# Kernel optimization log

Hardware: AMD Instinct MI355X
Metric: run time of the kernel (lower is better)

The kernel has to match this reference:

```python
import jax, jax.numpy as jnp
import numpy as np

N, F, H, C, E, K = 50000, 512, 512, 256, 800000, 1024


def _linear_params(key, fan_in, fan_out):
    kw, kb = jax.random.split(key)
    s = 1.0 / np.sqrt(fan_in)
    W = jax.random.uniform(kw, (fan_out, fan_in), jnp.float32, -s, s)
    b = jax.random.uniform(kb, (fan_out,), jnp.float32, -s, s)
    return W, b


def setup_inputs() -> dict:
    key = jax.random.key(0)
    ks = jax.random.split(key, 8)
    W1, b1 = _linear_params(ks[0], F, H)
    W2, b2 = _linear_params(ks[1], H, H)
    W3, b3 = _linear_params(ks[2], H, C)
    Wfc, bfc = _linear_params(ks[3], C, F)
    x = jax.random.normal(ks[4], (N, F), jnp.float32)
    edge_index = jax.random.randint(ks[5], (2, E), 0, N, jnp.int32)
    central_idx = jnp.sort(jax.random.randint(ks[6], (K,), 0, N, jnp.int32))
    zero = jnp.zeros((), jnp.float32)  # train_eps=True initialises eps=0
    return {
        "x": x, "edge_index": edge_index, "central_idx": central_idx,
        "W1": W1, "b1": b1, "eps1": zero,
        "W2": W2, "b2": b2, "eps2": zero,
        "W3": W3, "b3": b3, "eps3": zero,
        "Wfc": Wfc, "bfc": bfc,
    }


def _leaky_relu(v):
    return jnp.where(v >= 0, v, 0.2 * v)


def _gin_layer(h, edge_index, W, b, eps):
    # sum over neighbors (src -> dst); explicit self-loops add one extra h_i,
    # so total center coefficient is (1 + eps) + 1 = (2 + eps)
    n = h.shape[0]
    agg = jax.ops.segment_sum(h[edge_index[0]], edge_index[1], num_segments=n)
    return (agg + (2.0 + eps) * h) @ W.T + b


def reference(x, edge_index, central_idx, W1, b1, eps1, W2, b2, eps2,
              W3, b3, eps3, Wfc, bfc):
    h = _leaky_relu(_gin_layer(x, edge_index, W1, b1, eps1))
    h = _leaky_relu(_gin_layer(h, edge_index, W2, b2, eps2))
    x3 = _leaky_relu(_gin_layer(h, edge_index, W3, b3, eps3))
    # fc(x)[central_node_mask] == fc(x[central_idx]) for a mask with ones at central_idx
    out = x3[central_idx] @ Wfc.T + bfc
    return (x3, out)
```

## Files before the change

kernel.cpp:

```cpp
#include <hip/hip_runtime.h>
#include <stdint.h>

typedef unsigned short u16;
typedef __attribute__((ext_vector_type(4))) unsigned short u16x4;
typedef __attribute__((ext_vector_type(8))) unsigned short u16x8;
typedef __attribute__((ext_vector_type(8))) short bf16x8;
typedef __attribute__((ext_vector_type(4))) float f32x4;
typedef __attribute__((ext_vector_type(4))) float f4v;
typedef __attribute__((ext_vector_type(4))) int i32x4;

__device__ __forceinline__ float b2f(u16 u) {
    union { unsigned u; float f; } c; c.u = ((unsigned)u) << 16; return c.f;
}
__device__ __forceinline__ u16 f2b(float f) {
    union { float f; unsigned u; } c; c.f = f;
    unsigned r = c.u + 0x7fffu + ((c.u >> 16) & 1u);
    return (u16)(r >> 16);
}

__device__ __forceinline__ void gload16(const void* g, void* l) {
    __builtin_amdgcn_global_load_lds(
        (const __attribute__((address_space(1))) unsigned int*)g,
        (__attribute__((address_space(3))) unsigned int*)l, 16, 0, 0);
}

__device__ __forceinline__ void cvt4(const float* in, u16* out, int idx) {
    f4v v = ((const f4v*)in)[idx];
    u16x4 o;
    o[0] = f2b(v[0]); o[1] = f2b(v[1]); o[2] = f2b(v[2]); o[3] = f2b(v[3]);
    ((u16x4*)out)[idx] = o;
}

__device__ __forceinline__ float cvt_ub0(unsigned v) { float f; asm("v_cvt_f32_ubyte0 %0, %1" : "=v"(f) : "v"(v)); return f; }
__device__ __forceinline__ float cvt_ub1(unsigned v) { float f; asm("v_cvt_f32_ubyte1 %0, %1" : "=v"(f) : "v"(v)); return f; }
__device__ __forceinline__ float cvt_ub2(unsigned v) { float f; asm("v_cvt_f32_ubyte2 %0, %1" : "=v"(f) : "v"(v)); return f; }
__device__ __forceinline__ float cvt_ub3(unsigned v) { float f; asm("v_cvt_f32_ubyte3 %0, %1" : "=v"(f) : "v"(v)); return f; }

__device__ __forceinline__ void dq_accu(int2 d, float s, float* acc) {
    unsigned ux = (unsigned)d.x ^ 0x80808080u;
    unsigned uy = (unsigned)d.y ^ 0x80808080u;
    acc[0] = fmaf(s, cvt_ub0(ux), acc[0]);
    acc[1] = fmaf(s, cvt_ub1(ux), acc[1]);
    acc[2] = fmaf(s, cvt_ub2(ux), acc[2]);
    acc[3] = fmaf(s, cvt_ub3(ux), acc[3]);
    acc[4] = fmaf(s, cvt_ub0(uy), acc[4]);
    acc[5] = fmaf(s, cvt_ub1(uy), acc[5]);
    acc[6] = fmaf(s, cvt_ub2(uy), acc[6]);
    acc[7] = fmaf(s, cvt_ub3(uy), acc[7]);
}
__device__ __forceinline__ void dq_accu4(int d, float s, float* acc) {
    unsigned ux = (unsigned)d ^ 0x80808080u;
    acc[0] = fmaf(s, cvt_ub0(ux), acc[0]);
    acc[1] = fmaf(s, cvt_ub1(ux), acc[1]);
    acc[2] = fmaf(s, cvt_ub2(ux), acc[2]);
    acc[3] = fmaf(s, cvt_ub3(ux), acc[3]);
}

__device__ __forceinline__ void qrow512(const float* __restrict__ src, char* __restrict__ dst,
                                        float* __restrict__ srow, int r, int lane) {
    const f4v* p = (const f4v*)(src + (size_t)r * 512) + lane * 2;
    f4v v0 = p[0], v1 = p[1];
    float m = 0.f;
#pragma unroll
    for (int j = 0; j < 4; j++) { m = fmaxf(m, fabsf(v0[j])); m = fmaxf(m, fabsf(v1[j])); }
#pragma unroll
    for (int d = 1; d < 64; d <<= 1) m = fmaxf(m, __shfl_xor(m, d));
    float qs = (m > 0.f) ? 127.f / m : 0.f;
    int lo = 0, hi = 0;
#pragma unroll
    for (int j = 0; j < 4; j++) { int q = (int)rintf(v0[j] * qs); lo |= (q & 0xFF) << (8 * j); }
#pragma unroll
    for (int j = 0; j < 4; j++) { int q = (int)rintf(v1[j] * qs); hi |= (q & 0xFF) << (8 * j); }
    ((int2*)(dst + (size_t)r * 512))[lane] = make_int2(lo, hi);
    if (lane == 0) srow[r] = (m > 0.f) ? m / 127.f : 0.f;
}

__global__ void prep_kernel(const float* __restrict__ x, char* __restrict__ qx,
                            float* __restrict__ xs,
                            const float* __restrict__ W1, char* __restrict__ W1q, float* __restrict__ ws1,
                            const float* __restrict__ W2, char* __restrict__ W2q, float* __restrict__ ws2,
                            const float* __restrict__ W3, u16* __restrict__ W3b,
                            const int* __restrict__ ei, int* __restrict__ deg, int E) {
    int b = blockIdx.x;
    int tid = threadIdx.x;
    if (b < 12500) {
        int w = b * 4 + (tid >> 6);
        int lane = tid & 63;
        const f4v* xr = (const f4v*)(x + (size_t)w * 512) + lane * 2;
        f4v v0 = xr[0], v1 = xr[1];
        float m = 0.f;
#pragma unroll
        for (int j = 0; j < 4; j++) { m = fmaxf(m, fabsf(v0[j])); m = fmaxf(m, fabsf(v1[j])); }
#pragma unroll
        for (int d = 1; d < 8; d <<= 1) m = fmaxf(m, __shfl_xor(m, d));
        float scale = (m > 0.f) ? 127.f / m : 0.f;
        int lo = 0, hi = 0;
#pragma unroll
        for (int j = 0; j < 4; j++) { int q = (int)rintf(v0[j] * scale); lo |= (q & 0xFF) << (8 * j); }
#pragma unroll
        for (int j = 0; j < 4; j++) { int q = (int)rintf(v1[j] * scale); hi |= (q & 0xFF) << (8 * j); }
        ((int2*)(qx + (size_t)w * 512))[lane] = make_int2(lo, hi);
        if ((lane & 7) == 0) xs[w * 8 + (lane >> 3)] = (m > 0.f) ? m / 127.f : 0.f;
    } else if (b < 12628) {
        qrow512(W1, W1q, ws1, (b - 12500) * 4 + (tid >> 6), tid & 63);
    } else if (b < 12756) {
        qrow512(W2, W2q, ws2, (b - 12628) * 4 + (tid >> 6), tid & 63);
    } else if (b < 12884) {
        cvt4(W3, W3b, (b - 12756) * 256 + tid);
    } else {
        int e = (b - 12884) * 256 + tid;
        if (e < E) atomicAdd(&deg[ei[E + e]], 1);
    }
}

__global__ void scanA_kernel(const int* __restrict__ deg, int* __restrict__ bsum, int n) {
    __shared__ int sm[256];
    int tid = threadIdx.x;
    int i = blockIdx.x * 256 + tid;
    sm[tid] = (i < n) ? deg[i] : 0;
    __syncthreads();
#pragma unroll
    for (int off = 128; off > 0; off >>= 1) {
        if (tid < off) sm[tid] += sm[tid + off];
        __syncthreads();
    }
    if (tid == 0) bsum[blockIdx.x] = sm[0];
}

__global__ void scanB_kernel(int* __restrict__ bsum, int nb) {
    __shared__ int sm[256];
    int tid = threadIdx.x;
    int v = (tid < nb) ? bsum[tid] : 0;
    sm[tid] = v;
    __syncthreads();
#pragma unroll
    for (int off = 1; off < 256; off <<= 1) {
        int t = (tid >= off) ? sm[tid - off] : 0;
        __syncthreads();
        sm[tid] += t;
        __syncthreads();
    }
    if (tid < nb) bsum[tid] = sm[tid] - v;
}

__global__ void scanC_kernel(const int* __restrict__ deg, const int* __restrict__ bsum,
                             int* __restrict__ rowp, int n) {
    __shared__ int sm[256];
    int tid = threadIdx.x;
    int b = blockIdx.x;
    int i = b * 256 + tid;
    int v = (i < n) ? deg[i] : 0;
    sm[tid] = v;
    __syncthreads();
#pragma unroll
    for (int off = 1; off < 256; off <<= 1) {
        int t = (tid >= off) ? sm[tid - off] : 0;
        __syncthreads();
        sm[tid] += t;
        __syncthreads();
    }
    if (i < n) rowp[i] = bsum[b] + sm[tid] - v;
    if (i == n - 1) rowp[n] = bsum[b] + sm[tid];
}

__global__ void fill_kernel(const int* __restrict__ ei, const int* __restrict__ rowp,
                            int* __restrict__ cnt, int* __restrict__ col, int E) {
    int e = blockIdx.x * blockDim.x + threadIdx.x;
    if (e < E) {
        int dst = ei[E + e];
        int pos = atomicAdd(&cnt[dst], 1);
        col[rowp[dst] + pos] = ei[e];
    }
}

__global__ void agg_q512(const char* __restrict__ q, const float* __restrict__ sc,
                         char* __restrict__ tq, float* __restrict__ tsc,
                         const int* __restrict__ rowp, const int* __restrict__ col,
                         const float* __restrict__ epsp, int N) {
    int w = (blockIdx.x * blockDim.x + threadIdx.x) >> 6;
    if (w >= N) return;
    int lane = threadIdx.x & 63;
    float coef = 2.0f + epsp[0];
    const int2* base = (const int2*)q;
    int ch = lane >> 3;
    float acc[8];
#pragma unroll
    for (int j = 0; j < 8; j++) acc[j] = 0.f;
    float csum = 0.f;
    {
        float s = coef * sc[w * 8 + ch];
        csum += s;
        dq_accu(base[(size_t)w * 64 + lane], s, acc);
    }
    int p = rowp[w], e = rowp[w + 1];
    for (; p + 2 <= e; p += 2) {
        int s0 = __builtin_amdgcn_readfirstlane(col[p]);
        int s1 = __builtin_amdgcn_readfirstlane(col[p + 1]);
        int2 v0 = base[(size_t)s0 * 64 + lane];
        int2 v1 = base[(size_t)s1 * 64 + lane];
        float f0 = sc[s0 * 8 + ch];
        float f1 = sc[s1 * 8 + ch];
        csum += f0 + f1;
        dq_accu(v0, f0, acc);
        dq_accu(v1, f1, acc);
    }
    if (p < e) {
        int s0 = __builtin_amdgcn_readfirstlane(col[p]);
        float f0 = sc[s0 * 8 + ch];
        csum += f0;
        dq_accu(base[(size_t)s0 * 64 + lane], f0, acc);
    }
    float corr = 128.f * csum;
#pragma unroll
    for (int j = 0; j < 8; j++) acc[j] -= corr;
    float m = 0.f;
#pragma unroll
    for (int j = 0; j < 8; j++) m = fmaxf(m, fabsf(acc[j]));
#pragma unroll
    for (int d = 1; d < 64; d <<= 1) m = fmaxf(m, __shfl_xor(m, d));
    float qs = (m > 0.f) ? 127.f / m : 0.f;
    int lo = 0, hi = 0;
#pragma unroll
    for (int j = 0; j < 4; j++) { int qv = (int)rintf(acc[j] * qs); lo |= (qv & 0xFF) << (8 * j); }
#pragma unroll
    for (int j = 0; j < 4; j++) { int qv = (int)rintf(acc[j + 4] * qs); hi |= (qv & 0xFF) << (8 * j); }
    ((int2*)(tq + (size_t)w * 512))[lane] = make_int2(lo, hi);
    if (lane == 0) tsc[w] = (m > 0.f) ? m / 127.f : 0.f;
}

__global__ void agg3_q(const char* __restrict__ q, const float* __restrict__ sc,
                       float* __restrict__ out, const int* __restrict__ rowp,
                       const int* __restrict__ col, const float* __restrict__ epsp,
                       const float* __restrict__ bias, int N) {
    int w = (blockIdx.x * blockDim.x + threadIdx.x) >> 6;
    if (w >= N) return;
    int lane = threadIdx.x & 63;
    float coef = 2.0f + epsp[0];
    const int* base = (const int*)q;
    int ch = lane >> 4;
    f4v bv = *(const f4v*)(bias + lane * 4);
    float acc[4];
#pragma unroll
    for (int j = 0; j < 4; j++) acc[j] = 0.f;
    float csum = 0.f;
    {
        float s = coef * sc[w * 4 + ch];
        csum += s;
        dq_accu4(base[(size_t)w * 64 + lane], s, acc);
    }
    int p = rowp[w], e = rowp[w + 1];
    for (; p + 2 <= e; p += 2) {
        int s0 = __builtin_amdgcn_readfirstlane(col[p]);
        int s1 = __builtin_amdgcn_readfirstlane(col[p + 1]);
        int v0 = base[(size_t)s0 * 64 + lane];
        int v1 = base[(size_t)s1 * 64 + lane];
        float f0 = sc[s0 * 4 + ch];
        float f1 = sc[s1 * 4 + ch];
        csum += f0 + f1;
        dq_accu4(v0, f0, acc);
        dq_accu4(v1, f1, acc);
    }
    if (p < e) {
        int s0 = __builtin_amdgcn_readfirstlane(col[p]);
        float f0 = sc[s0 * 4 + ch];
        csum += f0;
        dq_accu4(base[(size_t)s0 * 64 + lane], f0, acc);
    }
    float corr = 128.f * csum;
    f4v o;
#pragma unroll
    for (int j = 0; j < 4; j++) {
        float v = acc[j] - corr + bv[j];
        o[j] = (v >= 0.f) ? v : 0.2f * v;
    }
    *(f4v*)(out + (size_t)w * 256 + lane * 4) = o;
}

template <int MODE>
__launch_bounds__(256)
__global__ void gemm_i8_kernel(const char* __restrict__ A, const float* __restrict__ sA,
                               const char* __restrict__ Wq, const float* __restrict__ sW,
                               const float* __restrict__ bias, u16* __restrict__ C,
                               char* __restrict__ qc, float* __restrict__ scw,
                               int M, int Nout, int K, int nby) {
    int nwg = gridDim.x;
    int orig = blockIdx.x;
    int q8 = nwg >> 3, r8 = nwg & 7;
    int xcd = orig & 7, idx = orig >> 3;
    int wgid = (xcd < r8 ? xcd * (q8 + 1) : r8 * (q8 + 1) + (xcd - r8) * q8) + idx;
    int by = wgid % nby;
    int bx = wgid / nby;

    __shared__ alignas(16) char lA[2][128 * 64];
    __shared__ alignas(16) char lB[2][128 * 64];
    int tid = threadIdx.x;
    int lane = tid & 63;
    int wv = tid >> 6;
    int m0 = bx * 128;
    int n0 = by * 128;
    int wrow = (wv >> 1) * 64;
    int wcol = (wv & 1) * 64;

    i32x4 acc[4][4];
#pragma unroll
    for (int i = 0; i < 4; i++)
#pragma unroll
        for (int j = 0; j < 4; j++) acc[i][j] = (i32x4){0, 0, 0, 0};

    int srow = lane >> 2;
    int scol = (lane & 3) * 16;
    int arow0 = m0 + wv * 16 + srow;        if (arow0 >= M) arow0 = M - 1;
    int arow1 = m0 + 64 + wv * 16 + srow;   if (arow1 >= M) arow1 = M - 1;
    const char* gA0 = A + (size_t)arow0 * K + scol;
    const char* gA1 = A + (size_t)arow1 * K + scol;
    const char* gB0 = Wq + (size_t)(n0 + wv * 16 + srow) * K + scol;
    const char* gB1 = Wq + (size_t)(n0 + 64 + wv * 16 + srow) * K + scol;
    int la0 = (wv * 16) * 64;
    int la1 = (64 + wv * 16) * 64;

    int fr = lane & 15;
    int kq = (lane >> 4) * 16;
    int nt = K / 64;

    gload16(gA0, lA[0] + la0);
    gload16(gA1, lA[0] + la1);
    gload16(gB0, lB[0] + la0);
    gload16(gB1, lB[0] + la1);
    __syncthreads();

    for (int t = 0; t < nt; t++) {
        int cur = t & 1;
        if (t + 1 < nt) {
            int kt = (t + 1) * 64;
            gload16(gA0 + kt, lA[cur ^ 1] + la0);
            gload16(gA1 + kt, lA[cur ^ 1] + la1);
            gload16(gB0 + kt, lB[cur ^ 1] + la0);
            gload16(gB1 + kt, lB[cur ^ 1] + la1);
        }
        i32x4 af[4], bf[4];
#pragma unroll
        for (int m = 0; m < 4; m++)
            af[m] = *(const i32x4*)(lA[cur] + (wrow + m * 16 + fr) * 64 + kq);
#pragma unroll
        for (int nf = 0; nf < 4; nf++)
            bf[nf] = *(const i32x4*)(lB[cur] + (wcol + nf * 16 + fr) * 64 + kq);
#pragma unroll
        for (int m = 0; m < 4; m++)
#pragma unroll
            for (int nf = 0; nf < 4; nf++)
                acc[m][nf] = __builtin_amdgcn_mfma_i32_16x16x64_i8(af[m], bf[nf], acc[m][nf], 0, 0, 0);
        __syncthreads();
    }

    int r0 = (lane >> 4) * 4;
#pragma unroll
    for (int m = 0; m < 4; m++) {
        float sa[4];
#pragma unroll
        for (int r = 0; r < 4; r++) {
            int gr = m0 + wrow + m * 16 + r0 + r;
            sa[r] = sA[gr < M ? gr : M - 1];
        }
        float v[4][4];
#pragma unroll
        for (int nf = 0; nf < 4; nf++) {
            int gc = n0 + wcol + nf * 16 + fr;
            float swv = sW[gc];
            float bv = bias[gc];
#pragma unroll
            for (int r = 0; r < 4; r++) {
                float tv = (float)acc[m][nf][r] * sa[r] * swv + bv;
                v[nf][r] = (tv >= 0.f) ? tv : 0.2f * tv;
            }
        }
        if constexpr (MODE == 1) {
#pragma unroll
            for (int nf = 0; nf < 4; nf++) {
                int gc = n0 + wcol + nf * 16 + fr;
#pragma unroll
                for (int r = 0; r < 4; r++) {
                    int gr = m0 + wrow + m * 16 + r0 + r;
                    if (gr < M) C[(size_t)gr * Nout + gc] = f2b(v[nf][r]);
                }
            }
        } else {
            int nch = Nout >> 6;
            int chunk = (n0 + wcol) >> 6;
#pragma unroll
            for (int r = 0; r < 4; r++) {
                float amax = fmaxf(fmaxf(fabsf(v[0][r]), fabsf(v[1][r])),
                                   fmaxf(fabsf(v[2][r]), fabsf(v[3][r])));
#pragma unroll
                for (int d = 1; d < 16; d <<= 1) amax = fmaxf(amax, __shfl_xor(amax, d));
                int gr = m0 + wrow + m * 16 + r0 + r;
                float scale = (amax > 0.f) ? 127.f / amax : 0.f;
                if (gr < M) {
#pragma unroll
                    for (int nf = 0; nf < 4; nf++) {
                        int qv = (int)rintf(v[nf][r] * scale);
                        qc[(size_t)gr * Nout + n0 + wcol + nf * 16 + fr] = (signed char)qv;
                    }
                    if (fr == 0)
                        scw[(size_t)gr * nch + chunk] = (amax > 0.f) ? amax / 127.f : 0.f;
                }
            }
        }
    }
}

#define BM 128
#define BN 128
#define BK 32

__launch_bounds__(256)
__global__ void gemm_bt_kernel(const u16* __restrict__ A, const u16* __restrict__ W,
                               char* __restrict__ qc, float* __restrict__ scw,
                               int M, int Nout, int K, int nby) {
    int nwg = gridDim.x;
    int orig = blockIdx.x;
    int q8 = nwg >> 3, r8 = nwg & 7;
    int xcd = orig & 7, idx = orig >> 3;
    int wgid = (xcd < r8 ? xcd * (q8 + 1) : r8 * (q8 + 1) + (xcd - r8) * q8) + idx;
    int by = wgid % nby;
    int bx = wgid / nby;

    __shared__ alignas(16) u16 lA[2][BM * BK];
    __shared__ alignas(16) u16 lB[2][BN * BK];
    int tid = threadIdx.x;
    int lane = tid & 63;
    int wv = tid >> 6;
    int m0 = bx * BM;
    int n0 = by * BN;
    int wrow = (wv >> 1) * 64;
    int wcol = (wv & 1) * 64;

    f32x4 acc[4][4];
#pragma unroll
    for (int i = 0; i < 4; i++)
#pragma unroll
        for (int j = 0; j < 4; j++) acc[i][j] = (f32x4){0.f, 0.f, 0.f, 0.f};

    int srow = lane >> 2;
    int scol = (lane & 3) * 8;
    int arow0 = m0 + wv * 16 + srow;        if (arow0 >= M) arow0 = M - 1;
    int arow1 = m0 + 64 + wv * 16 + srow;   if (arow1 >= M) arow1 = M - 1;
    const u16* gA0 = A + (size_t)arow0 * K + scol;
    const u16* gA1 = A + (size_t)arow1 * K + scol;
    const u16* gB0 = W + (size_t)(n0 + wv * 16 + srow) * K + scol;
    const u16* gB1 = W + (size_t)(n0 + 64 + wv * 16 + srow) * K + scol;
    int la0 = (wv * 16) * BK;
    int la1 = (64 + wv * 16) * BK;

    int fr = lane & 15;
    int kq = (lane >> 4) * 8;
    int nt = K / BK;

    gload16(gA0, lA[0] + la0);
    gload16(gA1, lA[0] + la1);
    gload16(gB0, lB[0] + la0);
    gload16(gB1, lB[0] + la1);
    __syncthreads();

    for (int t = 0; t < nt; t++) {
        int cur = t & 1;
        if (t + 1 < nt) {
            int kt = (t + 1) * BK;
            gload16(gA0 + kt, lA[cur ^ 1] + la0);
            gload16(gA1 + kt, lA[cur ^ 1] + la1);
            gload16(gB0 + kt, lB[cur ^ 1] + la0);
            gload16(gB1 + kt, lB[cur ^ 1] + la1);
        }
        bf16x8 af[4], bfr[4];
#pragma unroll
        for (int m = 0; m < 4; m++)
            af[m] = *(const bf16x8*)(lA[cur] + (wrow + m * 16 + fr) * BK + kq);
#pragma unroll
        for (int nf = 0; nf < 4; nf++)
            bfr[nf] = *(const bf16x8*)(lB[cur] + (wcol + nf * 16 + fr) * BK + kq);
#pragma unroll
        for (int m = 0; m < 4; m++)
#pragma unroll
            for (int nf = 0; nf < 4; nf++)
                acc[m][nf] = __builtin_amdgcn_mfma_f32_16x16x32_bf16(af[m], bfr[nf], acc[m][nf], 0, 0, 0);
        __syncthreads();
    }

    int r0 = (lane >> 4) * 4;
    int nch = Nout >> 6;
    int chunk = (n0 + wcol) >> 6;
#pragma unroll
    for (int m = 0; m < 4; m++) {
        float v[4][4];
#pragma unroll
        for (int nf = 0; nf < 4; nf++)
#pragma unroll
            for (int r = 0; r < 4; r++) v[nf][r] = acc[m][nf][r];
#pragma unroll
        for (int r = 0; r < 4; r++) {
            float amax = fmaxf(fmaxf(fabsf(v[0][r]), fabsf(v[1][r])),
                               fmaxf(fabsf(v[2][r]), fabsf(v[3][r])));
#pragma unroll
            for (int d = 1; d < 16; d <<= 1) amax = fmaxf(amax, __shfl_xor(amax, d));
            int gr = m0 + wrow + m * 16 + r0 + r;
            float scale = (amax > 0.f) ? 127.f / amax : 0.f;
            if (gr < M) {
#pragma unroll
                for (int nf = 0; nf < 4; nf++) {
                    int qv = (int)rintf(v[nf][r] * scale);
                    qc[(size_t)gr * Nout + n0 + wcol + nf * 16 + fr] = (signed char)qv;
                }
                if (fr == 0)
                    scw[(size_t)gr * nch + chunk] = (amax > 0.f) ? amax / 127.f : 0.f;
            }
        }
    }
}

__global__ void fc_kernel(const float* __restrict__ x3, const int* __restrict__ cidx,
                          const float* __restrict__ W, const float* __restrict__ b,
                          float* __restrict__ out, int C, int F, int Kc) {
    __shared__ float xr[8][256];
    int base = blockIdx.x * 8;
    int tid = threadIdx.x;
#pragma unroll
    for (int j = 0; j < 8; j++) {
        int k = base + j;
        if (k < Kc) xr[j][tid] = x3[(size_t)cidx[k] * C + tid];
    }
    __syncthreads();
    for (int f = tid; f < F; f += 256) {
        const float4* wr = (const float4*)(W + (size_t)f * C);
        float acc[8];
#pragma unroll
        for (int j = 0; j < 8; j++) acc[j] = 0.f;
        for (int c4 = 0; c4 < C / 4; ++c4) {
            float4 wv = wr[c4];
#pragma unroll
            for (int j = 0; j < 8; j++) {
                acc[j] += xr[j][c4 * 4 + 0] * wv.x + xr[j][c4 * 4 + 1] * wv.y +
                          xr[j][c4 * 4 + 2] * wv.z + xr[j][c4 * 4 + 3] * wv.w;
            }
        }
        float bf = b[f];
#pragma unroll
        for (int j = 0; j < 8; j++) {
            int k = base + j;
            if (k < Kc) out[(size_t)k * F + f] = acc[j] + bf;
        }
    }
}

extern "C" void kernel_launch(void* const* d_in, const int* in_sizes, int n_in,
                              void* d_out, int out_size, void* d_ws, size_t ws_size,
                              hipStream_t stream) {
    const float* x    = (const float*)d_in[0];
    const int*   ei   = (const int*)d_in[1];
    const int*   cidx = (const int*)d_in[2];
    const float* W1   = (const float*)d_in[3];
    const float* b1   = (const float*)d_in[4];
    const float* eps1 = (const float*)d_in[5];
    const float* W2   = (const float*)d_in[6];
    const float* b2   = (const float*)d_in[7];
    const float* eps2 = (const float*)d_in[8];
    const float* W3   = (const float*)d_in[9];
    const float* b3   = (const float*)d_in[10];
    const float* eps3 = (const float*)d_in[11];
    const float* Wfc  = (const float*)d_in[12];
    const float* bfc  = (const float*)d_in[13];

    const int F = 512, H = 512, Cc = 256;
    const int Nn = in_sizes[0] / F;
    const int E  = in_sizes[1] / 2;
    const int Kc = in_sizes[2];

    const size_t SZ_Q = (size_t)Nn * 512;
    char* ws = (char*)d_ws;
    char*  tq   = ws;
    char*  qbuf = ws + SZ_Q;
    float* tsc  = (float*)(ws + 2 * SZ_Q);
    float* sc   = tsc + Nn;
    char*  W1q  = (char*)(sc + (size_t)Nn * 8);
    float* ws1  = (float*)(W1q + 262144);
    char*  W2q  = (char*)(ws1 + 512);
    float* ws2  = (float*)(W2q + 262144);
    u16*   W3b  = (u16*)(ws2 + 512);
    int*   deg  = (int*)((char*)W3b + 262144);
    int*   cnt  = deg + Nn;
    int*   rowp = cnt + Nn;
    int*   colx = rowp + Nn + 1;
    int*   bsum = colx + E;

    u16* hbuf = (u16*)d_out;

    int nbScan = (Nn + 255) / 256;

    hipMemsetAsync(deg, 0, 2 * (size_t)Nn * sizeof(int), stream);
    int prepBlocks = 12884 + (E + 255) / 256;
    prep_kernel<<<prepBlocks, 256, 0, stream>>>(x, qbuf, sc, W1, W1q, ws1, W2, W2q, ws2,
                                                W3, W3b, ei, deg, E);
    scanA_kernel<<<nbScan, 256, 0, stream>>>(deg, bsum, Nn);
    scanB_kernel<<<1, 256, 0, stream>>>(bsum, nbScan);
    scanC_kernel<<<nbScan, 256, 0, stream>>>(deg, bsum, rowp, Nn);
    fill_kernel<<<(E + 255) / 256, 256, 0, stream>>>(ei, rowp, cnt, colx, E);

    int aggBlocks = (Nn * 64 + 255) / 256;
    int nbx = (Nn + 127) / 128;

    agg_q512<<<aggBlocks, 256, 0, stream>>>(qbuf, sc, tq, tsc, rowp, colx, eps1, Nn);
    gemm_i8_kernel<2><<<nbx * 4, 256, 0, stream>>>(tq, tsc, W1q, ws1, b1, nullptr,
                                                   qbuf, sc, Nn, H, F, 4);
    agg_q512<<<aggBlocks, 256, 0, stream>>>(qbuf, sc, tq, tsc, rowp, colx, eps2, Nn);
    gemm_i8_kernel<1><<<nbx * 4, 256, 0, stream>>>(tq, tsc, W2q, ws2, b2, hbuf,
                                                   nullptr, nullptr, Nn, H, H, 4);
    gemm_bt_kernel<<<nbx * 2, 256, 0, stream>>>(hbuf, W3b, qbuf, sc, Nn, Cc, H, 2);
    float* x3 = (float*)d_out;
    agg3_q<<<aggBlocks, 256, 0, stream>>>(qbuf, sc, x3, rowp, colx, eps3, b3, Nn);

    float* outp = x3 + (size_t)Nn * Cc;
    fc_kernel<<<(Kc + 7) / 8, 256, 0, stream>>>(x3, cidx, Wfc, bfc, outp, Cc, F, Kc);
}
```

Baseline: 451.5 us.

## Store quantized features in 64-column chunk planes and split aggregation per chunk

The int8 feature buffers move to a chunk-major layout: one plane of 64 columns per chunk, each row 64 bytes. Aggregation kernels launch one block slice per chunk, which shrinks the gather footprint per pass so it can stay cache-resident. Each wavefront also processes eight edges in parallel and reduces them with shuffles, instead of walking edges serially. The 512-wide aggregation now writes bf16 and needs a separate requantization kernel, which adds a pass and extra memory traffic. Edge-parallel lanes also waste work on padded slots when degree is low.

```diff
diff --git a/kernel.cpp b/kernel.cpp
--- a/kernel.cpp
+++ b/kernel.cpp
@@ -48,13 +48,6 @@
     acc[6] = fmaf(s, cvt_ub2(uy), acc[6]);
     acc[7] = fmaf(s, cvt_ub3(uy), acc[7]);
 }
-__device__ __forceinline__ void dq_accu4(int d, float s, float* acc) {
-    unsigned ux = (unsigned)d ^ 0x80808080u;
-    acc[0] = fmaf(s, cvt_ub0(ux), acc[0]);
-    acc[1] = fmaf(s, cvt_ub1(ux), acc[1]);
-    acc[2] = fmaf(s, cvt_ub2(ux), acc[2]);
-    acc[3] = fmaf(s, cvt_ub3(ux), acc[3]);
-}
 
 __device__ __forceinline__ void qrow512(const float* __restrict__ src, char* __restrict__ dst,
                                         float* __restrict__ srow, int r, int lane) {
@@ -75,12 +68,12 @@
     if (lane == 0) srow[r] = (m > 0.f) ? m / 127.f : 0.f;
 }
 
-__global__ void prep_kernel(const float* __restrict__ x, char* __restrict__ qx,
+__global__ void prep_kernel(const float* __restrict__ x, char* __restrict__ qxT,
                             float* __restrict__ xs,
                             const float* __restrict__ W1, char* __restrict__ W1q, float* __restrict__ ws1,
                             const float* __restrict__ W2, char* __restrict__ W2q, float* __restrict__ ws2,
                             const float* __restrict__ W3, u16* __restrict__ W3b,
-                            const int* __restrict__ ei, int* __restrict__ deg, int E) {
+                            const int* __restrict__ ei, int* __restrict__ deg, int E, int N) {
     int b = blockIdx.x;
     int tid = threadIdx.x;
     if (b < 12500) {
@@ -99,7 +92,7 @@
         for (int j = 0; j < 4; j++) { int q = (int)rintf(v0[j] * scale); lo |= (q & 0xFF) << (8 * j); }
 #pragma unroll
         for (int j = 0; j < 4; j++) { int q = (int)rintf(v1[j] * scale); hi |= (q & 0xFF) << (8 * j); }
-        ((int2*)(qx + (size_t)w * 512))[lane] = make_int2(lo, hi);
+        ((int2*)qxT)[((size_t)(lane >> 3) * N + w) * 8 + (lane & 7)] = make_int2(lo, hi);
         if ((lane & 7) == 0) xs[w * 8 + (lane >> 3)] = (m > 0.f) ? m / 127.f : 0.f;
     } else if (b < 12628) {
         qrow512(W1, W1q, ws1, (b - 12500) * 4 + (tid >> 6), tid & 63);
@@ -173,107 +166,126 @@
     }
 }
 
-__global__ void agg_q512(const char* __restrict__ q, const float* __restrict__ sc,
-                         char* __restrict__ tq, float* __restrict__ tsc,
-                         const int* __restrict__ rowp, const int* __restrict__ col,
-                         const float* __restrict__ epsp, int N) {
-    int w = (blockIdx.x * blockDim.x + threadIdx.x) >> 6;
+__global__ void agg_t512(const char* __restrict__ qT, const float* __restrict__ sc,
+                         u16* __restrict__ t, const int* __restrict__ rowp,
+                         const int* __restrict__ col, const float* __restrict__ epsp, int N) {
+    int tid = threadIdx.x;
+    int c = blockIdx.x & 7;
+    int w = (blockIdx.x >> 3) * 4 + (tid >> 6);
     if (w >= N) return;
-    int lane = threadIdx.x & 63;
+    int lane = tid & 63;
+    int slot = lane >> 3;
+    int fo = lane & 7;
+    const int2* plane = (const int2*)qT + (size_t)c * N * 8;
     float coef = 2.0f + epsp[0];
-    const int2* base = (const int2*)q;
-    int ch = lane >> 3;
     float acc[8];
 #pragma unroll
     for (int j = 0; j < 8; j++) acc[j] = 0.f;
     float csum = 0.f;
-    {
-        float s = coef * sc[w * 8 + ch];
+    if (slot == 0) {
+        float s = coef * sc[w * 8 + c];
         csum += s;
-        dq_accu(base[(size_t)w * 64 + lane], s, acc);
-    }
-    int p = rowp[w], e = rowp[w + 1];
-    for (; p + 2 <= e; p += 2) {
-        int s0 = __builtin_amdgcn_readfirstlane(col[p]);
-        int s1 = __builtin_amdgcn_readfirstlane(col[p + 1]);
-        int2 v0 = base[(size_t)s0 * 64 + lane];
-        int2 v1 = base[(size_t)s1 * 64 + lane];
-        float f0 = sc[s0 * 8 + ch];
-        float f1 = sc[s1 * 8 + ch];
-        csum += f0 + f1;
-        dq_accu(v0, f0, acc);
-        dq_accu(v1, f1, acc);
-    }
-    if (p < e) {
-        int s0 = __builtin_amdgcn_readfirstlane(col[p]);
-        float f0 = sc[s0 * 8 + ch];
-        csum += f0;
-        dq_accu(base[(size_t)s0 * 64 + lane], f0, acc);
-    }
-    float corr = 128.f * csum;
-#pragma unroll
-    for (int j = 0; j < 8; j++) acc[j] -= corr;
-    float m = 0.f;
-#pragma unroll
-    for (int j = 0; j < 8; j++) m = fmaxf(m, fabsf(acc[j]));
-#pragma unroll
-    for (int d = 1; d < 64; d <<= 1) m = fmaxf(m, __shfl_xor(m, d));
-    float qs = (m > 0.f) ? 127.f / m : 0.f;
-    int lo = 0, hi = 0;
-#pragma unroll
-    for (int j = 0; j < 4; j++) { int qv = (int)rintf(acc[j] * qs); lo |= (qv & 0xFF) << (8 * j); }
-#pragma unroll
-    for (int j = 0; j < 4; j++) { int qv = (int)rintf(acc[j + 4] * qs); hi |= (qv & 0xFF) << (8 * j); }
-    ((int2*)(tq + (size_t)w * 512))[lane] = make_int2(lo, hi);
-    if (lane == 0) tsc[w] = (m > 0.f) ? m / 127.f : 0.f;
-}
-
-__global__ void agg3_q(const char* __restrict__ q, const float* __restrict__ sc,
+        dq_accu(plane[(size_t)w * 8 + fo], s, acc);
+    }
+    int p0 = rowp[w], p1 = rowp[w + 1];
+    for (int p = p0; p < p1; p += 8) {
+        int e = p + slot;
+        int ec = (e < p1) ? e : p1 - 1;
+        int src = col[ec];
+        float s = (e < p1) ? sc[src * 8 + c] : 0.f;
+        csum += s;
+        dq_accu(plane[(size_t)src * 8 + fo], s, acc);
+    }
+#pragma unroll
+    for (int d = 8; d < 64; d <<= 1) {
+        csum += __shfl_xor(csum, d);
+#pragma unroll
+        for (int j = 0; j < 8; j++) acc[j] += __shfl_xor(acc[j], d);
+    }
+    if (slot == 0) {
+        float corr = 128.f * csum;
+        u16x8 o;
+#pragma unroll
+        for (int j = 0; j < 8; j++) o[j] = f2b(acc[j] - corr);
+        *(u16x8*)(t + (size_t)w * 512 + c * 64 + fo * 8) = o;
+    }
+}
+
+__global__ void agg3_t(const char* __restrict__ qT, const float* __restrict__ sc,
                        float* __restrict__ out, const int* __restrict__ rowp,
                        const int* __restrict__ col, const float* __restrict__ epsp,
                        const float* __restrict__ bias, int N) {
-    int w = (blockIdx.x * blockDim.x + threadIdx.x) >> 6;
+    int tid = threadIdx.x;
+    int x8 = blockIdx.x & 7;
+    int c = x8 >> 1;
+    int w = (blockIdx.x >> 3) * 8 + (x8 & 1) * 4 + (tid >> 6);
     if (w >= N) return;
+    int lane = tid & 63;
+    int slot = lane >> 3;
+    int fo = lane & 7;
+    const int2* plane = (const int2*)qT + (size_t)c * N * 8;
+    float coef = 2.0f + epsp[0];
+    float acc[8];
+#pragma unroll
+    for (int j = 0; j < 8; j++) acc[j] = 0.f;
+    float csum = 0.f;
+    if (slot == 0) {
+        float s = coef * sc[w * 4 + c];
+        csum += s;
+        dq_accu(plane[(size_t)w * 8 + fo], s, acc);
+    }
+    int p0 = rowp[w], p1 = rowp[w + 1];
+    for (int p = p0; p < p1; p += 8) {
+        int e = p + slot;
+        int ec = (e < p1) ? e : p1 - 1;
+        int src = col[ec];
+        float s = (e < p1) ? sc[src * 4 + c] : 0.f;
+        csum += s;
+        dq_accu(plane[(size_t)src * 8 + fo], s, acc);
+    }
+#pragma unroll
+    for (int d = 8; d < 64; d <<= 1) {
+        csum += __shfl_xor(csum, d);
+#pragma unroll
+        for (int j = 0; j < 8; j++) acc[j] += __shfl_xor(acc[j], d);
+    }
+    if (slot == 0) {
+        float corr = 128.f * csum;
+        int f0 = c * 64 + fo * 8;
+        f4v o0, o1;
+#pragma unroll
+        for (int j = 0; j < 4; j++) {
+            float v = acc[j] - corr + bias[f0 + j];
+            o0[j] = (v >= 0.f) ? v : 0.2f * v;
+        }
+#pragma unroll
+        for (int j = 0; j < 4; j++) {
+            float v = acc[j + 4] - corr + bias[f0 + 4 + j];
+            o1[j] = (v >= 0.f) ? v : 0.2f * v;
+        }
+        *(f4v*)(out + (size_t)w * 256 + f0) = o0;
+        *(f4v*)(out + (size_t)w * 256 + f0 + 4) = o1;
+    }
+}
+
+__global__ void requant512(const u16* __restrict__ h, char* __restrict__ qh,
+                           float* __restrict__ hs) {
+    int w = blockIdx.x * 4 + (threadIdx.x >> 6);
     int lane = threadIdx.x & 63;
-    float coef = 2.0f + epsp[0];
-    const int* base = (const int*)q;
-    int ch = lane >> 4;
-    f4v bv = *(const f4v*)(bias + lane * 4);
-    float acc[4];
-#pragma unroll
-    for (int j = 0; j < 4; j++) acc[j] = 0.f;
-    float csum = 0.f;
-    {
-        float s = coef * sc[w * 4 + ch];
-        csum += s;
-        dq_accu4(base[(size_t)w * 64 + lane], s, acc);
-    }
-    int p = rowp[w], e = rowp[w + 1];
-    for (; p + 2 <= e; p += 2) {
-        int s0 = __builtin_amdgcn_readfirstlane(col[p]);
-        int s1 = __builtin_amdgcn_readfirstlane(col[p + 1]);
-        int v0 = base[(size_t)s0 * 64 + lane];
-        int v1 = base[(size_t)s1 * 64 + lane];
-        float f0 = sc[s0 * 4 + ch];
-        float f1 = sc[s1 * 4 + ch];
-        csum += f0 + f1;
-        dq_accu4(v0, f0, acc);
-        dq_accu4(v1, f1, acc);
-    }
-    if (p < e) {
-        int s0 = __builtin_amdgcn_readfirstlane(col[p]);
-        float f0 = sc[s0 * 4 + ch];
-        csum += f0;
-        dq_accu4(base[(size_t)s0 * 64 + lane], f0, acc);
-    }
-    float corr = 128.f * csum;
-    f4v o;
-#pragma unroll
-    for (int j = 0; j < 4; j++) {
-        float v = acc[j] - corr + bv[j];
-        o[j] = (v >= 0.f) ? v : 0.2f * v;
-    }
-    *(f4v*)(out + (size_t)w * 256 + lane * 4) = o;
+    u16x8 v = ((const u16x8*)(h + (size_t)w * 512))[lane];
+    float f[8]; float m = 0.f;
+#pragma unroll
+    for (int j = 0; j < 8; j++) { f[j] = b2f(v[j]); m = fmaxf(m, fabsf(f[j])); }
+#pragma unroll
+    for (int d = 1; d < 64; d <<= 1) m = fmaxf(m, __shfl_xor(m, d));
+    float scale = (m > 0.f) ? 127.f / m : 0.f;
+    int lo = 0, hi = 0;
+#pragma unroll
+    for (int j = 0; j < 4; j++) { int q = (int)rintf(f[j] * scale); lo |= (q & 0xFF) << (8 * j); }
+#pragma unroll
+    for (int j = 0; j < 4; j++) { int q = (int)rintf(f[j + 4] * scale); hi |= (q & 0xFF) << (8 * j); }
+    ((int2*)(qh + (size_t)w * 512))[lane] = make_int2(lo, hi);
+    if (lane == 0) hs[w] = (m > 0.f) ? m / 127.f : 0.f;
 }
 
 template <int MODE>
@@ -398,7 +410,7 @@
 #pragma unroll
                     for (int nf = 0; nf < 4; nf++) {
                         int qv = (int)rintf(v[nf][r] * scale);
-                        qc[(size_t)gr * Nout + n0 + wcol + nf * 16 + fr] = (signed char)qv;
+                        qc[((size_t)chunk * M + gr) * 64 + (nf * 16 + fr)] = (signed char)qv;
                     }
                     if (fr == 0)
                         scw[(size_t)gr * nch + chunk] = (amax > 0.f) ? amax / 127.f : 0.f;
@@ -507,7 +519,7 @@
 #pragma unroll
                 for (int nf = 0; nf < 4; nf++) {
                     int qv = (int)rintf(v[nf][r] * scale);
-                    qc[(size_t)gr * Nout + n0 + wcol + nf * 16 + fr] = (signed char)qv;
+                    qc[((size_t)chunk * M + gr) * 64 + (nf * 16 + fr)] = (signed char)qv;
                 }
                 if (fr == 0)
                     scw[(size_t)gr * nch + chunk] = (amax > 0.f) ? amax / 127.f : 0.f;
@@ -575,9 +587,10 @@
 
     const size_t SZ_Q = (size_t)Nn * 512;
     char* ws = (char*)d_ws;
-    char*  tq   = ws;
-    char*  qbuf = ws + SZ_Q;
-    float* tsc  = (float*)(ws + 2 * SZ_Q);
+    u16*   bufT = (u16*)ws;
+    char*  tq   = ws + 2 * SZ_Q;
+    char*  qbuf = ws + 3 * SZ_Q;
+    float* tsc  = (float*)(ws + 4 * SZ_Q);
     float* sc   = tsc + Nn;
     char*  W1q  = (char*)(sc + (size_t)Nn * 8);
     float* ws1  = (float*)(W1q + 262144);
@@ -597,24 +610,27 @@
     hipMemsetAsync(deg, 0, 2 * (size_t)Nn * sizeof(int), stream);
     int prepBlocks = 12884 + (E + 255) / 256;
     prep_kernel<<<prepBlocks, 256, 0, stream>>>(x, qbuf, sc, W1, W1q, ws1, W2, W2q, ws2,
-                                                W3, W3b, ei, deg, E);
+                                                W3, W3b, ei, deg, E, Nn);
     scanA_kernel<<<nbScan, 256, 0, stream>>>(deg, bsum, Nn);
     scanB_kernel<<<1, 256, 0, stream>>>(bsum, nbScan);
     scanC_kernel<<<nbScan, 256, 0, stream>>>(deg, bsum, rowp, Nn);
     fill_kernel<<<(E + 255) / 256, 256, 0, stream>>>(ei, rowp, cnt, colx, E);
 
-    int aggBlocks = (Nn * 64 + 255) / 256;
+    int aggGrid = (Nn / 4) * 8;
+    int agg3Grid = (Nn / 8) * 8;
     int nbx = (Nn + 127) / 128;
 
-    agg_q512<<<aggBlocks, 256, 0, stream>>>(qbuf, sc, tq, tsc, rowp, colx, eps1, Nn);
+    agg_t512<<<aggGrid, 256, 0, stream>>>(qbuf, sc, bufT, rowp, colx, eps1, Nn);
+    requant512<<<Nn / 4, 256, 0, stream>>>(bufT, tq, tsc);
     gemm_i8_kernel<2><<<nbx * 4, 256, 0, stream>>>(tq, tsc, W1q, ws1, b1, nullptr,
                                                    qbuf, sc, Nn, H, F, 4);
-    agg_q512<<<aggBlocks, 256, 0, stream>>>(qbuf, sc, tq, tsc, rowp, colx, eps2, Nn);
+    agg_t512<<<aggGrid, 256, 0, stream>>>(qbuf, sc, bufT, rowp, colx, eps2, Nn);
+    requant512<<<Nn / 4, 256, 0, stream>>>(bufT, tq, tsc);
     gemm_i8_kernel<1><<<nbx * 4, 256, 0, stream>>>(tq, tsc, W2q, ws2, b2, hbuf,
                                                    nullptr, nullptr, Nn, H, H, 4);
     gemm_bt_kernel<<<nbx * 2, 256, 0, stream>>>(hbuf, W3b, qbuf, sc, Nn, Cc, H, 2);
     float* x3 = (float*)d_out;
-    agg3_q<<<aggBlocks, 256, 0, stream>>>(qbuf, sc, x3, rowp, colx, eps3, b3, Nn);
+    agg3_t<<<agg3Grid, 256, 0, stream>>>(qbuf, sc, x3, rowp, colx, eps3, b3, Nn);
 
     float* outp = x3 + (size_t)Nn * Cc;
     fc_kernel<<<(Kc + 7) / 8, 256, 0, stream>>>(x3, cidx, Wfc, bfc, outp, Cc, F, Kc);
```

Measured after the change: 794.1 us. +75.9%, slower.
